# Kernel optimization log

Measured on AMD Instinct MI355X. Metric: run time of the kernel, lower is better.

Reference implementation:

```python
import jax, jax.numpy as jnp
import numpy as np
import math

D_MODEL = 1024
N_HEADS = 16
D_K = 64
CHUNK_LEN = 64


def setup_inputs() -> dict:
    key = jax.random.key(0)
    ks = jax.random.split(key, 12)
    hd = N_HEADS * D_K
    s = 0.02
    return {
        'h': jax.random.normal(ks[0], (4, 2048, D_MODEL), jnp.float32),
        'e': jax.random.normal(ks[1], (4, 32, 2, 128, D_MODEL), jnp.float32),
        'Wq': jax.random.normal(ks[2], (D_MODEL, hd), jnp.float32) * s,
        'bq': jnp.zeros((hd,), jnp.float32),
        'Wk': jax.random.normal(ks[3], (D_MODEL, hd), jnp.float32) * s,
        'bk': jnp.zeros((hd,), jnp.float32),
        'Wv': jax.random.normal(ks[4], (D_MODEL, hd), jnp.float32) * s,
        'bv': jnp.zeros((hd,), jnp.float32),
        'Wo': jax.random.normal(ks[5], (hd, D_MODEL), jnp.float32) * s,
        'bo': jnp.zeros((D_MODEL,), jnp.float32),
        'gamma': jnp.ones((D_MODEL,), jnp.float32),
        'beta': jnp.zeros((D_MODEL,), jnp.float32),
    }


def reference(h, e, Wq, bq, Wk, bk, Wv, bv, Wo, bo, gamma, beta):
    b, chunks, neighbors, nlen, d_model = e.shape
    seq_len = h.shape[1]
    scale = 1.0 / math.sqrt(D_K)
    h_res = h
    # shift so chunk i attends to neighbors retrieved for chunk i
    hh = h[:, CHUNK_LEN - 1:]
    # layer norm
    mu = jnp.mean(hh, axis=-1, keepdims=True)
    var = jnp.mean(jnp.square(hh - mu), axis=-1, keepdims=True)
    hh = (hh - mu) / jnp.sqrt(var + 1e-5) * gamma + beta
    # pad to chunks * CHUNK_LEN
    pad = chunks * CHUNK_LEN - hh.shape[1]
    hh = jnp.pad(hh, ((0, 0), (0, pad), (0, 0)))
    hh = hh.reshape(b, chunks, CHUNK_LEN, d_model)
    q = (hh @ Wq + bq).reshape(b, chunks, CHUNK_LEN, N_HEADS, D_K)
    k = (e @ Wk + bk).reshape(b, chunks, neighbors, nlen, N_HEADS, D_K)
    v = (e @ Wv + bv).reshape(b, chunks, neighbors, nlen, N_HEADS, D_K)
    attn = jnp.einsum('bcihd,bcnjhd->bchinj', q, k) * scale  # [b,c,h,i,n,j]
    a_shape = attn.shape
    attn = jax.nn.softmax(attn.reshape(*a_shape[:-2], -1), axis=-1).reshape(a_shape)
    out = jnp.einsum('bchinj,bcnjhd->bcihd', attn, v)
    out = out.reshape(b, chunks * CHUNK_LEN, N_HEADS * D_K)
    out = out @ Wo + bo
    out = jnp.pad(out, ((0, 0), (CHUNK_LEN - 1, 0), (0, 0)))
    return out[:, :seq_len] + h_res
```

## Files before the change

kernel.cpp:

```cpp
#include <hip/hip_runtime.h>
#include <cstdint>
#include <cstddef>


typedef float f32x4 __attribute__((ext_vector_type(4)));
typedef __bf16 bf16x8 __attribute__((ext_vector_type(8)));

static __device__ __forceinline__ ushort f2bf(float f) {
  union { float f; uint32_t u; } x; x.f = f;
  uint32_t r = x.u + 0x7fffu + ((x.u >> 16) & 1u);
  return (ushort)(r >> 16);
}

static __device__ __forceinline__ bf16x8 ld_frag(const ushort* p) {
  union { uint4 u; bf16x8 v; } x;
  x.u = *(const uint4*)p;
  return x.v;
}

static __device__ __forceinline__ void gl2lds16(const ushort* g, ushort* l) {
  __builtin_amdgcn_global_load_lds(
      (const __attribute__((address_space(1))) void*)g,
      (__attribute__((address_space(3))) void*)l,
      16, 0, 0);
}

__global__ __launch_bounds__(256) void transpose_cast4(const float* __restrict__ Wq,
                                                       const float* __restrict__ Wk,
                                                       const float* __restrict__ Wv,
                                                       const float* __restrict__ Wo,
                                                       ushort* __restrict__ WqT,
                                                       ushort* __restrict__ WkvT,
                                                       ushort* __restrict__ WoT) {
  const float* W; ushort* WT;
  switch (blockIdx.z) {
    case 0:  W = Wq; WT = WqT; break;
    case 1:  W = Wk; WT = WkvT; break;
    case 2:  W = Wv; WT = WkvT + (size_t)1024 * 1024; break;
    default: W = Wo; WT = WoT; break;
  }
  __shared__ float tile[64][65];
  const int t = threadIdx.x;
  const int n0 = blockIdx.x * 64, k0 = blockIdx.y * 64;
#pragma unroll
  for (int i = 0; i < 4; ++i) {
    int lid = i * 256 + t;
    int r = lid >> 4, c4 = (lid & 15) * 4;
    float4 v = *(const float4*)&W[(size_t)(k0 + r) * 1024 + n0 + c4];
    tile[r][c4 + 0] = v.x; tile[r][c4 + 1] = v.y;
    tile[r][c4 + 2] = v.z; tile[r][c4 + 3] = v.w;
  }
  __syncthreads();
#pragma unroll
  for (int i = 0; i < 4; ++i) {
    int lid = i * 256 + t;
    int n = lid >> 4, k4 = (lid & 15) * 4;
    ushort4 o;
    o.x = f2bf(tile[k4 + 0][n]); o.y = f2bf(tile[k4 + 1][n]);
    o.z = f2bf(tile[k4 + 2][n]); o.w = f2bf(tile[k4 + 3][n]);
    *(ushort4*)&WT[(size_t)(n0 + n) * 1024 + k0 + k4] = o;
  }
}

__global__ __launch_bounds__(256) void cast_bf16(const float* __restrict__ x,
                                                 ushort* __restrict__ y) {
  const size_t i = ((size_t)blockIdx.x * 256 + threadIdx.x) * 8;
  float4 a = *(const float4*)&x[i];
  float4 b = *(const float4*)&x[i + 4];
  ushort o[8];
  o[0] = f2bf(a.x); o[1] = f2bf(a.y); o[2] = f2bf(a.z); o[3] = f2bf(a.w);
  o[4] = f2bf(b.x); o[5] = f2bf(b.y); o[6] = f2bf(b.z); o[7] = f2bf(b.w);
  *(uint4*)&y[i] = *(const uint4*)o;
}

__global__ __launch_bounds__(256) void ln_kernel(const float* __restrict__ h,
                                                 const float* __restrict__ gamma,
                                                 const float* __restrict__ beta,
                                                 ushort* __restrict__ hh) {
  const int bx = blockIdx.x;
  const int b = bx >> 11, s = bx & 2047;
  const int t = threadIdx.x;
  ushort* orow = hh + (size_t)(b * 2048 + s) * 1024;
  if (s >= 1985) {
    ushort4 z; z.x = 0; z.y = 0; z.z = 0; z.w = 0;
    *(ushort4*)&orow[t * 4] = z;
    return;
  }
  const float* xrow = h + (size_t)(b * 2048 + 63 + s) * 1024;
  float4 x = *(const float4*)&xrow[t * 4];
  float s1 = x.x + x.y + x.z + x.w;
  float s2 = x.x * x.x + x.y * x.y + x.z * x.z + x.w * x.w;
#pragma unroll
  for (int off = 32; off > 0; off >>= 1) {
    s1 += __shfl_xor(s1, off);
    s2 += __shfl_xor(s2, off);
  }
  __shared__ float a1[4], a2[4];
  if ((t & 63) == 0) { a1[t >> 6] = s1; a2[t >> 6] = s2; }
  __syncthreads();
  s1 = a1[0] + a1[1] + a1[2] + a1[3];
  s2 = a2[0] + a2[1] + a2[2] + a2[3];
  const float mu = s1 * (1.0f / 1024.0f);
  const float var = s2 * (1.0f / 1024.0f) - mu * mu;
  const float rstd = rsqrtf(var + 1e-5f);
  float4 g = *(const float4*)&gamma[t * 4];
  float4 be = *(const float4*)&beta[t * 4];
  ushort4 o;
  o.x = f2bf((x.x - mu) * rstd * g.x + be.x);
  o.y = f2bf((x.y - mu) * rstd * g.y + be.y);
  o.z = f2bf((x.z - mu) * rstd * g.z + be.z);
  o.w = f2bf((x.w - mu) * rstd * g.w + be.w);
  *(ushort4*)&orow[t * 4] = o;
}

template <int MODE, int NT>
__global__ __launch_bounds__(256) void gemm_bf16(const ushort* __restrict__ A,
                                                 const ushort* __restrict__ Bt,
                                                 const float* __restrict__ bias,
                                                 const float* __restrict__ bias2,
                                                 ushort* __restrict__ Cbf,
                                                 ushort* __restrict__ Vtg,
                                                 float* __restrict__ Cf,
                                                 const float* __restrict__ resid,
                                                 int mtiles, float scale) {
  __shared__ __align__(16) ushort Alds[128 * 32];
  __shared__ __align__(16) ushort Blds[128 * 32];
  const int t = threadIdx.x;
  const int lane = t & 63, wave = t >> 6;
  const int quad = lane >> 4, l16 = lane & 15;

  const int L = blockIdx.x;
  const int xcd = L & 7, slot = L >> 3;
  const int nt = slot & (NT - 1);
  const int mt = xcd * (mtiles >> 3) + (slot / NT);
  const int m0 = mt * 128, n0 = nt * 128;

  const int srow = lane >> 2;
  const int scol = (lane & 3) * 8;
  const int c0 = wave * 2;
  const ushort* gA0 = A  + (size_t)(m0 + c0 * 16 + srow) * 1024 + scol;
  const ushort* gA1 = gA0 + 16 * 1024;
  const ushort* gB0 = Bt + (size_t)(n0 + c0 * 16 + srow) * 1024 + scol;
  const ushort* gB1 = gB0 + 16 * 1024;
  ushort* dA0 = &Alds[c0 * 512 + lane * 8];
  ushort* dA1 = dA0 + 512;
  ushort* dB0 = &Blds[c0 * 512 + lane * 8];
  ushort* dB1 = dB0 + 512;

  const int wrow = (wave >> 1) * 64, wcol = (wave & 1) * 64;
  const ushort* pA = &Alds[(wrow + l16) * 32 + quad * 8];
  const ushort* pB = &Blds[(wcol + l16) * 32 + quad * 8];

  f32x4 zero = {0.f, 0.f, 0.f, 0.f};
  f32x4 acc[4][4];
#pragma unroll
  for (int i = 0; i < 4; ++i)
#pragma unroll
    for (int j = 0; j < 4; ++j) acc[i][j] = zero;

  for (int kb = 0; kb < 32; ++kb) {
    const int ko = kb * 32;
    gl2lds16(gA0 + ko, dA0);
    gl2lds16(gA1 + ko, dA1);
    gl2lds16(gB0 + ko, dB0);
    gl2lds16(gB1 + ko, dB1);
    __syncthreads();
    bf16x8 af[4], bfv[4];
#pragma unroll
    for (int i = 0; i < 4; ++i) af[i]  = ld_frag(pA + i * 16 * 32);
#pragma unroll
    for (int j = 0; j < 4; ++j) bfv[j] = ld_frag(pB + j * 16 * 32);
#pragma unroll
    for (int i = 0; i < 4; ++i)
#pragma unroll
      for (int j = 0; j < 4; ++j)
        acc[i][j] = __builtin_amdgcn_mfma_f32_16x16x32_bf16(af[i], bfv[j], acc[i][j], 0, 0, 0);
    __syncthreads();
  }

#pragma unroll
  for (int mi = 0; mi < 4; ++mi)
#pragma unroll
    for (int mj = 0; mj < 4; ++mj) {
      const int cc = n0 + wcol + mj * 16 + l16;
      const int r0 = m0 + wrow + mi * 16 + quad * 4;
      if constexpr (MODE == 0) {
        const float bvb = bias[cc];
#pragma unroll
        for (int rr = 0; rr < 4; ++rr)
          Cbf[(size_t)(r0 + rr) * 1024 + cc] = f2bf((acc[mi][mj][rr] + bvb) * scale);
      } else if constexpr (MODE == 2) {
        if (nt < 8) {
          const float bvb = bias[cc];
#pragma unroll
          for (int rr = 0; rr < 4; ++rr)
            Cbf[(size_t)(r0 + rr) * 1024 + cc] = f2bf(acc[mi][mj][rr] + bvb);
        } else {
          const int cv = cc - 1024;
          const int hh_ = cv >> 6, dd = cv & 63;
          const float bvb = bias2[cv];
          const int bcl = r0 >> 8, j0 = r0 & 255;
          ushort4 o;
          o.x = f2bf(acc[mi][mj][0] + bvb);
          o.y = f2bf(acc[mi][mj][1] + bvb);
          o.z = f2bf(acc[mi][mj][2] + bvb);
          o.w = f2bf(acc[mi][mj][3] + bvb);
          *(ushort4*)&Vtg[((size_t)(bcl * 16 + hh_)) * 16384 + dd * 256 + j0] = o;
        }
      } else {
        const float bvb = bias[cc];
#pragma unroll
        for (int rr = 0; rr < 4; ++rr) {
          const int r = r0 + rr;
          const int b = r >> 11, s = r & 2047;
          if (s < 1985) {
            const size_t o = (size_t)(b * 2048 + s + 63) * 1024 + cc;
            Cf[o] = acc[mi][mj][rr] + bvb + resid[o];
          }
        }
      }
    }
}

__global__ __launch_bounds__(256) void attn_kernel(const ushort* __restrict__ Qb,
                                                   const ushort* __restrict__ Kb,
                                                   const ushort* __restrict__ Vtg,
                                                   ushort* __restrict__ Ob) {
  __shared__ __align__(16) ushort smem[4608 + 18432 + 16896];
  __shared__ float redm[4][64];
  __shared__ float reds[4][64];
  ushort* Qs = smem;
  ushort* Ks = smem + 4608;
  ushort* Vt = smem + 23040;
  ushort* Ps = smem;

  const int t = threadIdx.x;
  const int bx = blockIdx.x;
  const int hd = bx & 15, c = (bx >> 4) & 31, b = bx >> 9;
  const int lane = t & 63, wave = t >> 6;
  const int quad = lane >> 4, l16 = lane & 15;

  const int qrow0 = b * 2048 + c * 64;
  const int kvrow0 = (b * 32 + c) * 256;
  const int colh = hd * 64;
  const ushort* vsrc = Vtg + ((size_t)((b * 32 + c) * 16 + hd)) * 16384;

#pragma unroll
  for (int it = 0; it < 2; ++it) {
    int lid = it * 256 + t;
    int r = lid >> 3, ch = (lid & 7) * 8;
    uint4 v = *(const uint4*)&Qb[(size_t)(qrow0 + r) * 1024 + colh + ch];
    *(uint4*)&Qs[r * 72 + ch] = v;
  }
#pragma unroll
  for (int it = 0; it < 8; ++it) {
    int lid = it * 256 + t;
    int r = lid >> 3, ch = (lid & 7) * 8;
    uint4 v = *(const uint4*)&Kb[(size_t)(kvrow0 + r) * 1024 + colh + ch];
    *(uint4*)&Ks[r * 72 + ch] = v;
  }
#pragma unroll
  for (int it = 0; it < 8; ++it) {
    int lid = it * 256 + t;
    int row = lid >> 5, c8 = (lid & 31) * 8;
    uint4 v = *(const uint4*)&vsrc[row * 256 + c8];
    *(uint4*)&Vt[row * 264 + c8] = v;
  }
  __syncthreads();

  const int jw = wave * 64;
  f32x4 zero = {0.f, 0.f, 0.f, 0.f};
  f32x4 acc[4][4];
#pragma unroll
  for (int i = 0; i < 4; ++i)
#pragma unroll
    for (int j = 0; j < 4; ++j) acc[i][j] = zero;

#pragma unroll
  for (int kb = 0; kb < 2; ++kb) {
    bf16x8 af[4], bfv[4];
#pragma unroll
    for (int mi = 0; mi < 4; ++mi)
      af[mi] = ld_frag(&Qs[(mi * 16 + l16) * 72 + kb * 32 + quad * 8]);
#pragma unroll
    for (int mj = 0; mj < 4; ++mj)
      bfv[mj] = ld_frag(&Ks[(jw + mj * 16 + l16) * 72 + kb * 32 + quad * 8]);
#pragma unroll
    for (int mi = 0; mi < 4; ++mi)
#pragma unroll
      for (int mj = 0; mj < 4; ++mj)
        acc[mi][mj] = __builtin_amdgcn_mfma_f32_16x16x32_bf16(af[mi], bfv[mj], acc[mi][mj], 0, 0, 0);
  }

  float rmax[4][4];
#pragma unroll
  for (int mi = 0; mi < 4; ++mi)
#pragma unroll
    for (int rr = 0; rr < 4; ++rr) {
      float m = fmaxf(fmaxf(acc[mi][0][rr], acc[mi][1][rr]),
                      fmaxf(acc[mi][2][rr], acc[mi][3][rr]));
      m = fmaxf(m, __shfl_xor(m, 1));
      m = fmaxf(m, __shfl_xor(m, 2));
      m = fmaxf(m, __shfl_xor(m, 4));
      m = fmaxf(m, __shfl_xor(m, 8));
      rmax[mi][rr] = m;
    }
  if (l16 == 0) {
#pragma unroll
    for (int mi = 0; mi < 4; ++mi)
#pragma unroll
      for (int rr = 0; rr < 4; ++rr)
        redm[wave][mi * 16 + quad * 4 + rr] = rmax[mi][rr];
  }
  __syncthreads();
  float gmax[4][4];
#pragma unroll
  for (int mi = 0; mi < 4; ++mi)
#pragma unroll
    for (int rr = 0; rr < 4; ++rr) {
      const int row = mi * 16 + quad * 4 + rr;
      gmax[mi][rr] = fmaxf(fmaxf(redm[0][row], redm[1][row]),
                           fmaxf(redm[2][row], redm[3][row]));
    }
  float rsum[4][4];
#pragma unroll
  for (int mi = 0; mi < 4; ++mi)
#pragma unroll
    for (int rr = 0; rr < 4; ++rr) {
      float s = 0.f;
#pragma unroll
      for (int mj = 0; mj < 4; ++mj) {
        float p = exp2f((acc[mi][mj][rr] - gmax[mi][rr]) * 1.4426950408889634f);
        acc[mi][mj][rr] = p;
        s += p;
      }
      s += __shfl_xor(s, 1);
      s += __shfl_xor(s, 2);
      s += __shfl_xor(s, 4);
      s += __shfl_xor(s, 8);
      rsum[mi][rr] = s;
    }
  if (l16 == 0) {
#pragma unroll
    for (int mi = 0; mi < 4; ++mi)
#pragma unroll
      for (int rr = 0; rr < 4; ++rr)
        reds[wave][mi * 16 + quad * 4 + rr] = rsum[mi][rr];
  }
  __syncthreads();
#pragma unroll
  for (int mi = 0; mi < 4; ++mi)
#pragma unroll
    for (int rr = 0; rr < 4; ++rr) {
      const int row = mi * 16 + quad * 4 + rr;
      const float inv = 1.0f / (reds[0][row] + reds[1][row] + reds[2][row] + reds[3][row]);
#pragma unroll
      for (int mj = 0; mj < 4; ++mj)
        Ps[row * 264 + jw + mj * 16 + l16] = f2bf(acc[mi][mj][rr] * inv);
    }
  __syncthreads();

  const int d0 = wave * 16;
  f32x4 acc2[4];
#pragma unroll
  for (int mi = 0; mi < 4; ++mi) acc2[mi] = zero;
#pragma unroll
  for (int kb = 0; kb < 8; ++kb) {
    bf16x8 bfv = ld_frag(&Vt[(d0 + l16) * 264 + kb * 32 + quad * 8]);
#pragma unroll
    for (int mi = 0; mi < 4; ++mi) {
      bf16x8 af = ld_frag(&Ps[(mi * 16 + l16) * 264 + kb * 32 + quad * 8]);
      acc2[mi] = __builtin_amdgcn_mfma_f32_16x16x32_bf16(af, bfv, acc2[mi], 0, 0, 0);
    }
  }
#pragma unroll
  for (int mi = 0; mi < 4; ++mi)
#pragma unroll
    for (int rr = 0; rr < 4; ++rr) {
      const int i = mi * 16 + quad * 4 + rr;
      Ob[(size_t)(qrow0 + i) * 1024 + colh + d0 + l16] = f2bf(acc2[mi][rr]);
    }
}

__global__ __launch_bounds__(256) void head_copy(const float* __restrict__ h,
                                                 float* __restrict__ out) {
  const int idx4 = blockIdx.x * 256 + threadIdx.x;
  const int b = idx4 / 16128;
  const int rem = idx4 - b * 16128;
  const size_t o = (size_t)b * 2048 * 1024 + (size_t)rem * 4;
  *(float4*)&out[o] = *(const float4*)&h[o];
}

extern "C" void kernel_launch(void* const* d_in, const int* in_sizes, int n_in,
                              void* d_out, int out_size, void* d_ws, size_t ws_size,
                              hipStream_t stream) {
  const float* h     = (const float*)d_in[0];
  const float* e     = (const float*)d_in[1];
  const float* Wq    = (const float*)d_in[2];
  const float* bq    = (const float*)d_in[3];
  const float* Wk    = (const float*)d_in[4];
  const float* bk    = (const float*)d_in[5];
  const float* Wv    = (const float*)d_in[6];
  const float* bv    = (const float*)d_in[7];
  const float* Wo    = (const float*)d_in[8];
  const float* bo    = (const float*)d_in[9];
  const float* gamma = (const float*)d_in[10];
  const float* beta  = (const float*)d_in[11];
  float* out = (float*)d_out;

  char* ws = (char*)d_ws;
  ushort* WqT  = (ushort*)(ws + ((size_t)0 << 20));
  ushort* WkvT = (ushort*)(ws + ((size_t)2 << 20));
  ushort* WoT  = (ushort*)(ws + ((size_t)6 << 20));
  ushort* hhb  = (ushort*)(ws + ((size_t)8 << 20));
  ushort* Qb   = (ushort*)(ws + ((size_t)24 << 20));
  ushort* Kb   = (ushort*)(ws + ((size_t)40 << 20));
  ushort* VtG  = (ushort*)(ws + ((size_t)104 << 20));
  ushort* Ob   = (ushort*)(ws + ((size_t)168 << 20));

  transpose_cast4<<<dim3(16, 16, 4), 256, 0, stream>>>(Wq, Wk, Wv, Wo, WqT, WkvT, WoT);

  ln_kernel<<<8192, 256, 0, stream>>>(h, gamma, beta, hhb);

  gemm_bf16<0, 8><<<512, 256, 0, stream>>>(hhb, WqT, bq, nullptr, Qb, nullptr,
                                           nullptr, nullptr, 64, 0.125f);

  for (int q = 0; q < 4; ++q) {
    const size_t roff = (size_t)q * 8192 * 1024;
    cast_bf16<<<4096, 256, 0, stream>>>(e + roff, hhb);
    gemm_bf16<2, 16><<<1024, 256, 0, stream>>>(hhb, WkvT, bk, bv, Kb + roff,
                                               VtG + roff, nullptr, nullptr, 64, 1.0f);
  }

  attn_kernel<<<2048, 256, 0, stream>>>(Qb, Kb, VtG, Ob);

  gemm_bf16<1, 8><<<512, 256, 0, stream>>>(Ob, WoT, bo, nullptr, nullptr, nullptr,
                                           out, h, 64, 1.0f);
  head_copy<<<252, 256, 0, stream>>>(h, out);
}
```

Measured before the change: 605.6 us.

## Double K-step per barrier in bf16 GEMM and halve KV projection launches

The GEMM main loop now loads two 32-wide K slices into separate LDS buffers per iteration, halving the number of barrier pairs per tile at the cost of twice the LDS footprint. The K/V projection runs as two larger launches instead of four, with a row offset parameter so V-transpose output indexing stays correct. Workspace buffers are reorganised so one staging buffer is reused for LN output, cast inputs and attention output. The larger LDS use may lower occupancy.

```diff
diff --git a/kernel.cpp b/kernel.cpp
--- a/kernel.cpp
+++ b/kernel.cpp
@@ -122,9 +122,10 @@
                                                  ushort* __restrict__ Vtg,
                                                  float* __restrict__ Cf,
                                                  const float* __restrict__ resid,
-                                                 int mtiles, float scale) {
-  __shared__ __align__(16) ushort Alds[128 * 32];
-  __shared__ __align__(16) ushort Blds[128 * 32];
+                                                 int mtiles, float scale,
+                                                 int mrow_off) {
+  __shared__ __align__(16) ushort Alds[2][128 * 32];
+  __shared__ __align__(16) ushort Blds[2][128 * 32];
   const int t = threadIdx.x;
   const int lane = t & 63, wave = t >> 6;
   const int quad = lane >> 4, l16 = lane & 15;
@@ -142,14 +143,15 @@
   const ushort* gA1 = gA0 + 16 * 1024;
   const ushort* gB0 = Bt + (size_t)(n0 + c0 * 16 + srow) * 1024 + scol;
   const ushort* gB1 = gB0 + 16 * 1024;
-  ushort* dA0 = &Alds[c0 * 512 + lane * 8];
+  ushort* dA0 = &Alds[0][c0 * 512 + lane * 8];
   ushort* dA1 = dA0 + 512;
-  ushort* dB0 = &Blds[c0 * 512 + lane * 8];
+  ushort* dB0 = &Blds[0][c0 * 512 + lane * 8];
   ushort* dB1 = dB0 + 512;
+  const ptrdiff_t SUB = 128 * 32;
 
   const int wrow = (wave >> 1) * 64, wcol = (wave & 1) * 64;
-  const ushort* pA = &Alds[(wrow + l16) * 32 + quad * 8];
-  const ushort* pB = &Blds[(wcol + l16) * 32 + quad * 8];
+  const ushort* pA = &Alds[0][(wrow + l16) * 32 + quad * 8];
+  const ushort* pB = &Blds[0][(wcol + l16) * 32 + quad * 8];
 
   f32x4 zero = {0.f, 0.f, 0.f, 0.f};
   f32x4 acc[4][4];
@@ -158,23 +160,26 @@
 #pragma unroll
     for (int j = 0; j < 4; ++j) acc[i][j] = zero;
 
-  for (int kb = 0; kb < 32; ++kb) {
-    const int ko = kb * 32;
-    gl2lds16(gA0 + ko, dA0);
-    gl2lds16(gA1 + ko, dA1);
-    gl2lds16(gB0 + ko, dB0);
-    gl2lds16(gB1 + ko, dB1);
+  for (int kb = 0; kb < 16; ++kb) {
+    const int ko = kb * 64;
+    gl2lds16(gA0 + ko, dA0);         gl2lds16(gA1 + ko, dA1);
+    gl2lds16(gA0 + ko + 32, dA0 + SUB); gl2lds16(gA1 + ko + 32, dA1 + SUB);
+    gl2lds16(gB0 + ko, dB0);         gl2lds16(gB1 + ko, dB1);
+    gl2lds16(gB0 + ko + 32, dB0 + SUB); gl2lds16(gB1 + ko + 32, dB1 + SUB);
     __syncthreads();
-    bf16x8 af[4], bfv[4];
-#pragma unroll
-    for (int i = 0; i < 4; ++i) af[i]  = ld_frag(pA + i * 16 * 32);
-#pragma unroll
-    for (int j = 0; j < 4; ++j) bfv[j] = ld_frag(pB + j * 16 * 32);
-#pragma unroll
-    for (int i = 0; i < 4; ++i)
-#pragma unroll
-      for (int j = 0; j < 4; ++j)
-        acc[i][j] = __builtin_amdgcn_mfma_f32_16x16x32_bf16(af[i], bfv[j], acc[i][j], 0, 0, 0);
+#pragma unroll
+    for (int sub = 0; sub < 2; ++sub) {
+      bf16x8 af[4], bfv[4];
+#pragma unroll
+      for (int i = 0; i < 4; ++i) af[i]  = ld_frag(pA + sub * SUB + i * 512);
+#pragma unroll
+      for (int j = 0; j < 4; ++j) bfv[j] = ld_frag(pB + sub * SUB + j * 512);
+#pragma unroll
+      for (int i = 0; i < 4; ++i)
+#pragma unroll
+        for (int j = 0; j < 4; ++j)
+          acc[i][j] = __builtin_amdgcn_mfma_f32_16x16x32_bf16(af[i], bfv[j], acc[i][j], 0, 0, 0);
+    }
     __syncthreads();
   }
 
@@ -199,7 +204,8 @@
           const int cv = cc - 1024;
           const int hh_ = cv >> 6, dd = cv & 63;
           const float bvb = bias2[cv];
-          const int bcl = r0 >> 8, j0 = r0 & 255;
+          const int gr0 = r0 + mrow_off;
+          const int bcl = gr0 >> 8, j0 = gr0 & 255;
           ushort4 o;
           o.x = f2bf(acc[mi][mj][0] + bvb);
           o.y = f2bf(acc[mi][mj][1] + bvb);
@@ -409,32 +415,32 @@
   float* out = (float*)d_out;
 
   char* ws = (char*)d_ws;
-  ushort* WqT  = (ushort*)(ws + ((size_t)0 << 20));
-  ushort* WkvT = (ushort*)(ws + ((size_t)2 << 20));
-  ushort* WoT  = (ushort*)(ws + ((size_t)6 << 20));
-  ushort* hhb  = (ushort*)(ws + ((size_t)8 << 20));
-  ushort* Qb   = (ushort*)(ws + ((size_t)24 << 20));
-  ushort* Kb   = (ushort*)(ws + ((size_t)40 << 20));
-  ushort* VtG  = (ushort*)(ws + ((size_t)104 << 20));
-  ushort* Ob   = (ushort*)(ws + ((size_t)168 << 20));
+  ushort* stg  = (ushort*)(ws + ((size_t)0 << 20));
+  ushort* WqT  = (ushort*)(ws + ((size_t)32 << 20));
+  ushort* WkvT = (ushort*)(ws + ((size_t)34 << 20));
+  ushort* WoT  = (ushort*)(ws + ((size_t)38 << 20));
+  ushort* Qb   = (ushort*)(ws + ((size_t)40 << 20));
+  ushort* Kb   = (ushort*)(ws + ((size_t)56 << 20));
+  ushort* VtG  = (ushort*)(ws + ((size_t)120 << 20));
 
   transpose_cast4<<<dim3(16, 16, 4), 256, 0, stream>>>(Wq, Wk, Wv, Wo, WqT, WkvT, WoT);
 
-  ln_kernel<<<8192, 256, 0, stream>>>(h, gamma, beta, hhb);
-
-  gemm_bf16<0, 8><<<512, 256, 0, stream>>>(hhb, WqT, bq, nullptr, Qb, nullptr,
-                                           nullptr, nullptr, 64, 0.125f);
-
-  for (int q = 0; q < 4; ++q) {
-    const size_t roff = (size_t)q * 8192 * 1024;
-    cast_bf16<<<4096, 256, 0, stream>>>(e + roff, hhb);
-    gemm_bf16<2, 16><<<1024, 256, 0, stream>>>(hhb, WkvT, bk, bv, Kb + roff,
-                                               VtG + roff, nullptr, nullptr, 64, 1.0f);
-  }
-
-  attn_kernel<<<2048, 256, 0, stream>>>(Qb, Kb, VtG, Ob);
-
-  gemm_bf16<1, 8><<<512, 256, 0, stream>>>(Ob, WoT, bo, nullptr, nullptr, nullptr,
-                                           out, h, 64, 1.0f);
+  ln_kernel<<<8192, 256, 0, stream>>>(h, gamma, beta, stg);
+
+  gemm_bf16<0, 8><<<512, 256, 0, stream>>>(stg, WqT, bq, nullptr, Qb, nullptr,
+                                           nullptr, nullptr, 64, 0.125f, 0);
+
+  for (int half = 0; half < 2; ++half) {
+    const size_t roff = (size_t)half * 16384 * 1024;
+    cast_bf16<<<8192, 256, 0, stream>>>(e + roff, stg);
+    gemm_bf16<2, 16><<<2048, 256, 0, stream>>>(stg, WkvT, bk, bv, Kb + roff,
+                                               VtG, nullptr, nullptr,
+                                               128, 1.0f, half * 16384);
+  }
+
+  attn_kernel<<<2048, 256, 0, stream>>>(Qb, Kb, VtG, stg);
+
+  gemm_bf16<1, 8><<<512, 256, 0, stream>>>(stg, WoT, bo, nullptr, nullptr, nullptr,
+                                           out, h, 64, 1.0f, 0);
   head_copy<<<252, 256, 0, stream>>>(h, out);
 }
```

Measured after the change: 566.3 us. -6.5%, faster.
